# Kernel optimization log

Hardware: AMD Instinct MI355X
Metric: run time of the kernel (lower is better)

The kernel has to match this reference:

```python
import jax, jax.numpy as jnp
import numpy as np

GAMMA = 0.99
GAE_LAMBDA = 0.95
CLIP = 0.2
ENT_COEF = 0.01
VF_COEF = 0.5


def setup_inputs() -> dict:
    key = jax.random.key(0)
    ks = jax.random.split(key, 12)
    T, D, H, A = 65536, 512, 256, 16
    obs = jax.random.normal(ks[0], (T, D), dtype=jnp.float32)
    actions = jax.random.randint(ks[1], (T,), 0, A, dtype=jnp.int32)
    logprobs = jax.random.normal(ks[2], (T,), dtype=jnp.float32)
    rewards = jax.random.normal(ks[3], (T,), dtype=jnp.float32)
    terms = jax.random.uniform(ks[4], (T,), dtype=jnp.float32)
    values = jax.random.normal(ks[5], (T,), dtype=jnp.float32)
    # orthogonal-init-like scaling (std sqrt(2) for trunk, 0.01 actor, 1.0 critic)
    W1 = jax.random.normal(ks[6], (D, H), dtype=jnp.float32) * np.float32(np.sqrt(2.0 / D))
    b1 = jnp.zeros((H,), jnp.float32)
    W2 = jax.random.normal(ks[7], (H, H), dtype=jnp.float32) * np.float32(np.sqrt(2.0 / H))
    b2 = jnp.zeros((H,), jnp.float32)
    Wa = jax.random.normal(ks[8], (H, A), dtype=jnp.float32) * np.float32(0.01 / np.sqrt(H))
    ba = jnp.zeros((A,), jnp.float32)
    Wc = jax.random.normal(ks[9], (H, 1), dtype=jnp.float32) * np.float32(1.0 / np.sqrt(H))
    bc = jnp.zeros((1,), jnp.float32)
    return {"obs": obs, "actions": actions, "logprobs": logprobs, "rewards": rewards,
            "terms": terms, "values": values, "W1": W1, "b1": b1, "W2": W2, "b2": b2,
            "Wa": Wa, "ba": ba, "Wc": Wc, "bc": bc}


def reference(obs, actions, logprobs, rewards, terms, values,
              W1, b1, W2, b2, Wa, ba, Wc, bc):
    # ---- GAE (torch.no_grad in original -> stop_gradient) ----
    nonterm = 1.0 - terms                                   # [T]
    next_vals = jnp.concatenate([values[1:], jnp.zeros((1,), values.dtype)])
    delta = rewards + GAMMA * next_vals * nonterm - values  # [T]

    def step(carry, x):  # reverse recurrence a_t = d_t + g*l*nt_t * a_{t+1}
        d, nt = x
        g = d + GAMMA * GAE_LAMBDA * nt * carry
        return g, g

    _, adv = jax.lax.scan(step, jnp.float32(0.0), (delta, nonterm), reverse=True)
    adv = jax.lax.stop_gradient(adv)
    returns = adv + jax.lax.stop_gradient(values)
    vals_old = jax.lax.stop_gradient(values)

    # ---- actor-critic MLP (get_action_and_value) ----
    hidden = jnp.tanh(jnp.tanh(obs @ W1 + b1) @ W2 + b2)    # [T,256]
    logits = hidden @ Wa + ba                               # [T,A]
    logp = jax.nn.log_softmax(logits, axis=-1)
    newlp = jnp.take_along_axis(logp, actions[:, None].astype(jnp.int32), axis=1)[:, 0]
    entropy = -jnp.sum(jnp.exp(logp) * logp, axis=-1)       # [T]
    value = (hidden @ Wc + bc)[:, 0]                        # [T]

    # ---- clipped PPO losses (single full-batch minibatch) ----
    ratio = jnp.exp(newlp - logprobs)
    a = (adv - adv.mean()) / (adv.std() + 1e-8)
    pg_loss = jnp.maximum(-a * ratio, -a * jnp.clip(ratio, 1.0 - CLIP, 1.0 + CLIP)).mean()
    v_clipped = vals_old + jnp.clip(value - vals_old, -CLIP, CLIP)
    v_loss = 0.5 * jnp.maximum((value - returns) ** 2, (v_clipped - returns) ** 2).mean()
    loss = pg_loss - ENT_COEF * entropy.mean() + VF_COEF * v_loss
    return loss
```

## Files before the change

kernel.cpp:

```cpp
#include <hip/hip_runtime.h>


#define TT 65536

typedef float f32x4 __attribute__((ext_vector_type(4)));
typedef __bf16 bf16x8 __attribute__((ext_vector_type(8)));
typedef unsigned short u16x8 __attribute__((ext_vector_type(8)));
typedef unsigned int u32x4 __attribute__((ext_vector_type(4)));

__device__ __forceinline__ unsigned short f2bf(float f) {
    unsigned int u = __float_as_uint(f);
    unsigned int r = (u + 0x7fffu + ((u >> 16) & 1u)) >> 16;
    return (unsigned short)r;
}

__device__ __forceinline__ unsigned int cvt_pk_bf16(float a, float b) {
    unsigned int r;
    asm("v_cvt_pk_bf16_f32 %0, %1, %2" : "=v"(r) : "v"(a), "v"(b));
    return r;
}

__device__ __forceinline__ float fast_tanh(float x) {
    float e = __expf(2.0f * x);
    return fmaf(-2.0f, __builtin_amdgcn_rcpf(e + 1.0f), 1.0f);
}

__device__ __forceinline__ void lds_barrier() {
    asm volatile("s_waitcnt lgkmcnt(0)" ::: "memory");
    __builtin_amdgcn_s_barrier();
}

__device__ __forceinline__ void suffix_scan256(float* sC, float* sD, int i) {
    float c = sC[i], d = sD[i];
#pragma unroll
    for (int s = 1; s < 256; s <<= 1) {
        float c2 = 1.0f, d2 = 0.0f;
        if (i + s < 256) { c2 = sC[i + s]; d2 = sD[i + s]; }
        __syncthreads();
        d = d + c * d2;
        c = c * c2;
        sC[i] = c; sD[i] = d;
        __syncthreads();
    }
}

__device__ __forceinline__ void gae_cd(const float* rewards, const float* terms,
                                       const float* values, int t, float* c, float* d) {
    float nt = 1.0f - terms[t];
    float nv = (t + 1 < TT) ? values[t + 1] : 0.0f;
    *d = rewards[t] + 0.99f * nv * nt - values[t];
    *c = 0.99f * 0.95f * nt;
}

__global__ void k_prep_gae1(const float* __restrict__ W1, const float* __restrict__ W2,
                            const float* __restrict__ Wa, const float* __restrict__ Wc,
                            unsigned short* __restrict__ W1Tf, unsigned short* __restrict__ W2Tf,
                            unsigned short* __restrict__ Wavf,
                            const float* __restrict__ rewards, const float* __restrict__ terms,
                            const float* __restrict__ values, float* __restrict__ aggC,
                            float* __restrict__ aggD) {
    if (blockIdx.x < 800) {
        int idx = blockIdx.x * 256 + threadIdx.x;
        if (idx < 131072) {
            int e = idx & 7, l = (idx >> 3) & 63, nt = (idx >> 9) & 15, kt = idx >> 13;
            int col = nt * 16 + (l & 15);
            int k = kt * 32 + ((l >> 4) << 3) + e;
            W1Tf[idx] = f2bf(W1[k * 256 + col]);
        } else if (idx < 196608) {
            int i = idx - 131072;
            int e = i & 7, l = (i >> 3) & 63, nt = (i >> 9) & 15, kt = i >> 13;
            int col = nt * 16 + (l & 15);
            int k = kt * 32 + ((l >> 4) << 3) + e;
            W2Tf[i] = f2bf(W2[k * 256 + col]);
        } else if (idx < 204800) {
            int i = idx - 196608;
            int e = i & 7, l = (i >> 3) & 63, h = (i >> 9) & 1, kt = i >> 10;
            int k = kt * 32 + ((l >> 4) << 3) + e;
            int a = l & 15;
            float v = (h == 0) ? Wa[k * 16 + a] : ((a == 0) ? Wc[k] : 0.0f);
            Wavf[i] = f2bf(v);
        }
        return;
    }
    __shared__ float sC[256], sD[256];
    int i = threadIdx.x;
    int b = blockIdx.x - 800;
    int t = b * 256 + i;
    float c, d;
    gae_cd(rewards, terms, values, t, &c, &d);
    sC[i] = c; sD[i] = d;
    __syncthreads();
    suffix_scan256(sC, sD, i);
    if (i == 0) { aggC[b] = sC[0]; aggD[b] = sD[0]; }
}

__global__ void k_gae3(const float* __restrict__ rewards, const float* __restrict__ terms,
                       const float* __restrict__ values, const float* __restrict__ aggC,
                       const float* __restrict__ aggD, float* __restrict__ adv,
                       float* __restrict__ ret, float* __restrict__ sumP) {
    __shared__ float sC[256], sD[256];
    int i = threadIdx.x, b = blockIdx.x;
    sC[i] = aggC[i]; sD[i] = aggD[i];
    __syncthreads();
    suffix_scan256(sC, sD, i);
    float carry = (b < 255) ? sD[b + 1] : 0.0f;
    __syncthreads();

    int t = b * 256 + i;
    float c, d;
    gae_cd(rewards, terms, values, t, &c, &d);
    sC[i] = c; sD[i] = d;
    __syncthreads();
    suffix_scan256(sC, sD, i);
    float a = sD[i] + sC[i] * carry;
    adv[t] = a;
    ret[t] = a + values[t];
    __syncthreads();
    sC[i] = a; sD[i] = a * a;
    __syncthreads();
#pragma unroll
    for (int s = 128; s > 0; s >>= 1) {
        if (i < s) { sC[i] += sC[i + s]; sD[i] += sD[i + s]; }
        __syncthreads();
    }
    if (i == 0) { sumP[2 * b] = sC[0]; sumP[2 * b + 1] = sD[0]; }
}

__global__ void k_gae4(const float* __restrict__ sumP, float* __restrict__ stats) {
    __shared__ float s1[256], s2[256];
    int i = threadIdx.x;
    s1[i] = sumP[2 * i]; s2[i] = sumP[2 * i + 1];
    __syncthreads();
#pragma unroll
    for (int s = 128; s > 0; s >>= 1) {
        if (i < s) { s1[i] += s1[i + s]; s2[i] += s2[i + s]; }
        __syncthreads();
    }
    if (i == 0) {
        float mean = s1[0] * (1.0f / TT);
        float var = s2[0] * (1.0f / TT) - mean * mean;
        stats[0] = mean;
        stats[1] = 1.0f / (sqrtf(fmaxf(var, 0.0f)) + 1e-8f);
    }
}

__global__ __launch_bounds__(256, 3) void k_mlp(
    const float* __restrict__ obs, const int* __restrict__ actions,
    const float* __restrict__ logprobs, const float* __restrict__ values,
    const float* __restrict__ b1, const float* __restrict__ b2,
    const float* __restrict__ ba, const float* __restrict__ bc,
    const unsigned short* __restrict__ W1Tf, const unsigned short* __restrict__ W2Tf,
    const unsigned short* __restrict__ Wavf, const float* __restrict__ adv,
    const float* __restrict__ ret, const float* __restrict__ stats,
    float* __restrict__ lossP) {
    __shared__ __align__(16) unsigned char SM[40960];
    unsigned short* smA = (unsigned short*)SM;
    unsigned short* smH = (unsigned short*)(SM + 8192);

    const int tid = threadIdx.x;
    const int wid = tid >> 6;
    const int lane = tid & 63;
    const int cl = lane & 15;
    const int gg = lane >> 4;
    const int bm0 = blockIdx.x * 64;

    const int arow = tid >> 2;
    const int aslot = tid & 3;
    const int adst = arow * 32 + ((aslot ^ ((arow >> 1) & 3)) << 3);
    const float* aSrc = obs + (size_t)(bm0 + arow) * 512 + aslot * 8;

    const float meanA = stats[0], rstdA = stats[1];

    float b1v[4], b2v[4];
#pragma unroll
    for (int n = 0; n < 4; ++n) {
        int c = wid * 64 + n * 16 + cl;
        b1v[n] = b1[c];
        b2v[n] = b2[c];
    }
    const float bav = ba[cl];
    const float bc0 = bc[0];

    f32x4 acc[4][4];
#pragma unroll
    for (int m = 0; m < 4; ++m)
#pragma unroll
        for (int n = 0; n < 4; ++n) acc[m][n] = (f32x4){0.f, 0.f, 0.f, 0.f};

    auto cvtWriteA = [&](const float4& f0, const float4& f1, int buf) {
        u32x4 pk;
        pk[0] = cvt_pk_bf16(f0.x, f0.y);
        pk[1] = cvt_pk_bf16(f0.z, f0.w);
        pk[2] = cvt_pk_bf16(f1.x, f1.y);
        pk[3] = cvt_pk_bf16(f1.z, f1.w);
        *(u32x4*)&smA[buf * 2048 + adst] = pk;
    };

    {
        const unsigned short* bBase = W1Tf + ((size_t)(wid * 4) << 9) + lane * 8;
        float4 pa0[3], pa1[3];
#pragma unroll
        for (int p = 0; p < 3; ++p) {
            pa0[p] = *(const float4*)(aSrc + p * 32);
            pa1[p] = *(const float4*)(aSrc + p * 32 + 4);
        }
        cvtWriteA(pa0[0], pa1[0], 0);
        lds_barrier();
#pragma unroll
        for (int t = 0; t < 16; ++t) {
            if (t < 13) {
                pa0[t % 3] = *(const float4*)(aSrc + (t + 3) * 32);
                pa1[t % 3] = *(const float4*)(aSrc + (t + 3) * 32 + 4);
            }
            bf16x8 av[4], bv[4];
#pragma unroll
            for (int n = 0; n < 4; ++n)
                bv[n] = *(const bf16x8*)(bBase + ((size_t)(t * 16 + n) << 9));
#pragma unroll
            for (int m = 0; m < 4; ++m) {
                int ra = m * 16 + cl;
                av[m] = *(const bf16x8*)&smA[(t & 1) * 2048 + ra * 32 + ((gg ^ ((ra >> 1) & 3)) << 3)];
            }
#pragma unroll
            for (int m = 0; m < 4; ++m)
#pragma unroll
                for (int n = 0; n < 4; ++n)
                    acc[m][n] = __builtin_amdgcn_mfma_f32_16x16x32_bf16(av[m], bv[n], acc[m][n], 0, 0, 0);
            if (t < 15) cvtWriteA(pa0[(t + 1) % 3], pa1[(t + 1) % 3], (t + 1) & 1);
            lds_barrier();
        }
    }

#pragma unroll
    for (int m = 0; m < 4; ++m)
#pragma unroll
        for (int n = 0; n < 4; ++n)
#pragma unroll
            for (int j = 0; j < 4; ++j) {
                int r = m * 16 + gg * 4 + j;
                int c = wid * 64 + n * 16 + cl;
                smH[r * 256 + (c ^ ((r & 7) << 3))] = f2bf(fast_tanh(acc[m][n][j] + b1v[n]));
                acc[m][n][j] = 0.0f;
            }
    __syncthreads();

    {
        const unsigned short* bBase = W2Tf + ((size_t)(wid * 4) << 9) + lane * 8;
#pragma unroll
        for (int t = 0; t < 8; ++t) {
            bf16x8 av[4], bv[4];
#pragma unroll
            for (int n = 0; n < 4; ++n)
                bv[n] = *(const bf16x8*)(bBase + ((size_t)(t * 16 + n) << 9));
#pragma unroll
            for (int m = 0; m < 4; ++m) {
                int ra = m * 16 + cl;
                av[m] = *(const bf16x8*)&smH[ra * 256 + ((t * 32 + gg * 8) ^ ((ra & 7) << 3))];
            }
#pragma unroll
            for (int m = 0; m < 4; ++m)
#pragma unroll
                for (int n = 0; n < 4; ++n)
                    acc[m][n] = __builtin_amdgcn_mfma_f32_16x16x32_bf16(av[m], bv[n], acc[m][n], 0, 0, 0);
        }
    }

    __syncthreads();
#pragma unroll
    for (int m = 0; m < 4; ++m)
#pragma unroll
        for (int n = 0; n < 4; ++n)
#pragma unroll
            for (int j = 0; j < 4; ++j) {
                int r = m * 16 + gg * 4 + j;
                int c = wid * 64 + n * 16 + cl;
                smH[r * 256 + (c ^ ((r & 7) << 3))] = f2bf(fast_tanh(acc[m][n][j] + b2v[n]));
            }
    __syncthreads();

    float lsum = 0.0f;
    {
        f32x4 acc_a = {0.f, 0.f, 0.f, 0.f}, acc_v = {0.f, 0.f, 0.f, 0.f};
        const unsigned short* wBase = Wavf + lane * 8;
#pragma unroll
        for (int kk = 0; kk < 8; ++kk) {
            int r = wid * 16 + cl;
            bf16x8 av = *(const bf16x8*)&smH[r * 256 + ((kk * 32 + gg * 8) ^ ((r & 7) << 3))];
            bf16x8 bva = *(const bf16x8*)(wBase + ((size_t)(kk * 2) << 9));
            bf16x8 bvv = *(const bf16x8*)(wBase + ((size_t)(kk * 2 + 1) << 9));
            acc_a = __builtin_amdgcn_mfma_f32_16x16x32_bf16(av, bva, acc_a, 0, 0, 0);
            acc_v = __builtin_amdgcn_mfma_f32_16x16x32_bf16(av, bvv, acc_v, 0, 0, 0);
        }

        const int t0 = bm0 + wid * 16;
#pragma unroll
        for (int j = 0; j < 4; ++j) {
            int t = t0 + gg * 4 + j;
            float lg = acc_a[j] + bav;
            float mx = lg;
#pragma unroll
            for (int dd = 1; dd < 16; dd <<= 1) mx = fmaxf(mx, __shfl_xor(mx, dd));
            float ex = __expf(lg - mx);
            float se = ex;
#pragma unroll
            for (int dd = 1; dd < 16; dd <<= 1) se += __shfl_xor(se, dd);
            float ls = __logf(se);
            float lp = lg - mx - ls;
            float pl = __expf(lp) * lp;
            float ent = pl;
#pragma unroll
            for (int dd = 1; dd < 16; dd <<= 1) ent += __shfl_xor(ent, dd);
            ent = -ent;
            int act = actions[t];
            float newlp = __shfl(lp, (lane & 48) | act);
            float val = __shfl(acc_v[j], lane & 48) + bc0;

            float lpo = logprobs[t];
            float at = (adv[t] - meanA) * rstdA;
            float rt = ret[t];
            float vo = values[t];
            float ratio = __expf(newlp - lpo);
            float rcl = fminf(fmaxf(ratio, 0.8f), 1.2f);
            float pg = fmaxf(-at * ratio, -at * rcl);
            float vcl = vo + fminf(fmaxf(val - vo, -0.2f), 0.2f);
            float dv = val - rt, dvc = vcl - rt;
            float vl = fmaxf(dv * dv, dvc * dvc);
            if (cl == 0) lsum += pg - 0.01f * ent + 0.25f * vl;
        }
        lsum += __shfl_xor(lsum, 16);
        lsum += __shfl_xor(lsum, 32);
    }
    __syncthreads();
    float* red2 = (float*)SM;
    if (lane == 0) red2[wid] = lsum;
    __syncthreads();
    if (tid == 0) lossP[blockIdx.x] = red2[0] + red2[1] + red2[2] + red2[3];
}

__global__ void k_final(const float* __restrict__ lossP, float* __restrict__ out) {
    __shared__ float s[256];
    int i = threadIdx.x;
    s[i] = lossP[i] + lossP[i + 256] + lossP[i + 512] + lossP[i + 768];
    __syncthreads();
#pragma unroll
    for (int st = 128; st > 0; st >>= 1) {
        if (i < st) s[i] += s[i + st];
        __syncthreads();
    }
    if (i == 0) out[0] = s[0] * (1.0f / TT);
}

extern "C" void kernel_launch(void* const* d_in, const int* in_sizes, int n_in,
                              void* d_out, int out_size, void* d_ws, size_t ws_size,
                              hipStream_t stream) {
    const float* obs      = (const float*)d_in[0];
    const int*   actions  = (const int*)d_in[1];
    const float* logprobs = (const float*)d_in[2];
    const float* rewards  = (const float*)d_in[3];
    const float* terms    = (const float*)d_in[4];
    const float* values   = (const float*)d_in[5];
    const float* W1 = (const float*)d_in[6];
    const float* b1 = (const float*)d_in[7];
    const float* W2 = (const float*)d_in[8];
    const float* b2 = (const float*)d_in[9];
    const float* Wa = (const float*)d_in[10];
    const float* ba = (const float*)d_in[11];
    const float* Wc = (const float*)d_in[12];
    const float* bc = (const float*)d_in[13];

    char* ws = (char*)d_ws;
    unsigned short* W1Tf = (unsigned short*)(ws + 0);
    unsigned short* W2Tf = (unsigned short*)(ws + 262144);
    unsigned short* Wavf = (unsigned short*)(ws + 393216);
    float* advp  = (float*)(ws + 409600);
    float* retp  = (float*)(ws + 671744);
    float* aggC  = (float*)(ws + 933888);
    float* aggD  = (float*)(ws + 934912);
    float* sumP  = (float*)(ws + 936960);
    float* stats = (float*)(ws + 939008);
    float* lossP = (float*)(ws + 939072);

    k_prep_gae1<<<1056, 256, 0, stream>>>(W1, W2, Wa, Wc, W1Tf, W2Tf, Wavf,
                                          rewards, terms, values, aggC, aggD);
    k_gae3<<<256, 256, 0, stream>>>(rewards, terms, values, aggC, aggD, advp, retp, sumP);
    k_gae4<<<1, 256, 0, stream>>>(sumP, stats);
    k_mlp<<<1024, 256, 0, stream>>>(obs, actions, logprobs, values, b1, b2, ba, bc,
                                    W1Tf, W2Tf, Wavf, advp, retp, stats, lossP);
    k_final<<<1, 256, 0, stream>>>(lossP, (float*)d_out);
}
```

Baseline: 73.42 us.

## Stage full obs tile in LDS upfront and prefetch first weight tiles

```diff
diff --git a/kernel.cpp b/kernel.cpp
--- a/kernel.cpp
+++ b/kernel.cpp
@@ -62,23 +62,29 @@
     if (blockIdx.x < 800) {
         int idx = blockIdx.x * 256 + threadIdx.x;
         if (idx < 131072) {
-            int e = idx & 7, l = (idx >> 3) & 63, nt = (idx >> 9) & 15, kt = idx >> 13;
-            int col = nt * 16 + (l & 15);
-            int k = kt * 32 + ((l >> 4) << 3) + e;
-            W1Tf[idx] = f2bf(W1[k * 256 + col]);
+            int col = idx & 255, k = idx >> 8;
+            int kt = k >> 5, lh = (k & 31) >> 3, e = k & 7;
+            int nt = col >> 4, cl = col & 15;
+            W1Tf[(((kt * 16 + nt) * 64) + lh * 16 + cl) * 8 + e] = f2bf(W1[k * 256 + col]);
         } else if (idx < 196608) {
             int i = idx - 131072;
-            int e = i & 7, l = (i >> 3) & 63, nt = (i >> 9) & 15, kt = i >> 13;
-            int col = nt * 16 + (l & 15);
-            int k = kt * 32 + ((l >> 4) << 3) + e;
-            W2Tf[i] = f2bf(W2[k * 256 + col]);
+            int col = i & 255, k = i >> 8;
+            int kt = k >> 5, lh = (k & 31) >> 3, e = k & 7;
+            int nt = col >> 4, cl = col & 15;
+            W2Tf[(((kt * 16 + nt) * 64) + lh * 16 + cl) * 8 + e] = f2bf(W2[k * 256 + col]);
         } else if (idx < 204800) {
             int i = idx - 196608;
-            int e = i & 7, l = (i >> 3) & 63, h = (i >> 9) & 1, kt = i >> 10;
-            int k = kt * 32 + ((l >> 4) << 3) + e;
-            int a = l & 15;
-            float v = (h == 0) ? Wa[k * 16 + a] : ((a == 0) ? Wc[k] : 0.0f);
-            Wavf[i] = f2bf(v);
+            if (i < 4096) {
+                int a = i & 15, k = i >> 4;
+                int kt = k >> 5, lh = (k & 31) >> 3, e = k & 7;
+                Wavf[(((kt * 2 + 0) * 64) + lh * 16 + a) * 8 + e] = f2bf(Wa[k * 16 + a]);
+            } else {
+                int j = i - 4096;
+                int a = j & 15, k = j >> 4;
+                int kt = k >> 5, lh = (k & 31) >> 3, e = k & 7;
+                float v = (a == 0) ? Wc[k] : 0.0f;
+                Wavf[(((kt * 2 + 1) * 64) + lh * 16 + a) * 8 + e] = f2bf(v);
+            }
         }
         return;
     }
@@ -144,7 +150,7 @@
     }
 }
 
-__global__ __launch_bounds__(256, 3) void k_mlp(
+__global__ __launch_bounds__(256, 2) void k_mlp(
     const float* __restrict__ obs, const int* __restrict__ actions,
     const float* __restrict__ logprobs, const float* __restrict__ values,
     const float* __restrict__ b1, const float* __restrict__ b2,
@@ -153,9 +159,9 @@
     const unsigned short* __restrict__ Wavf, const float* __restrict__ adv,
     const float* __restrict__ ret, const float* __restrict__ stats,
     float* __restrict__ lossP) {
-    __shared__ __align__(16) unsigned char SM[40960];
+    __shared__ __align__(16) unsigned char SM[65536];
     unsigned short* smA = (unsigned short*)SM;
-    unsigned short* smH = (unsigned short*)(SM + 8192);
+    unsigned short* smH = (unsigned short*)SM;
 
     const int tid = threadIdx.x;
     const int wid = tid >> 6;
@@ -164,11 +170,6 @@
     const int gg = lane >> 4;
     const int bm0 = blockIdx.x * 64;
 
-    const int arow = tid >> 2;
-    const int aslot = tid & 3;
-    const int adst = arow * 32 + ((aslot ^ ((arow >> 1) & 3)) << 3);
-    const float* aSrc = obs + (size_t)(bm0 + arow) * 512 + aslot * 8;
-
     const float meanA = stats[0], rstdA = stats[1];
 
     float b1v[4], b2v[4];
@@ -181,55 +182,64 @@
     const float bav = ba[cl];
     const float bc0 = bc[0];
 
+    {
+        const int arow = tid >> 2;
+        const int acl4 = (tid & 3) * 8;
+        const int axor = (arow & 7) << 3;
+        const float* aSrc = obs + (size_t)(bm0 + arow) * 512 + acl4;
+        unsigned short* aDst = smA + arow * 512;
+#pragma unroll
+        for (int ct = 0; ct < 16; ++ct) {
+            float4 f0 = *(const float4*)(aSrc + ct * 32);
+            float4 f1 = *(const float4*)(aSrc + ct * 32 + 4);
+            u32x4 pk;
+            pk[0] = cvt_pk_bf16(f0.x, f0.y);
+            pk[1] = cvt_pk_bf16(f0.z, f0.w);
+            pk[2] = cvt_pk_bf16(f1.x, f1.y);
+            pk[3] = cvt_pk_bf16(f1.z, f1.w);
+            *(u32x4*)&aDst[(ct * 32 + acl4) ^ axor] = pk;
+        }
+    }
+
     f32x4 acc[4][4];
 #pragma unroll
     for (int m = 0; m < 4; ++m)
 #pragma unroll
         for (int n = 0; n < 4; ++n) acc[m][n] = (f32x4){0.f, 0.f, 0.f, 0.f};
 
-    auto cvtWriteA = [&](const float4& f0, const float4& f1, int buf) {
-        u32x4 pk;
-        pk[0] = cvt_pk_bf16(f0.x, f0.y);
-        pk[1] = cvt_pk_bf16(f0.z, f0.w);
-        pk[2] = cvt_pk_bf16(f1.x, f1.y);
-        pk[3] = cvt_pk_bf16(f1.z, f1.w);
-        *(u32x4*)&smA[buf * 2048 + adst] = pk;
-    };
-
-    {
-        const unsigned short* bBase = W1Tf + ((size_t)(wid * 4) << 9) + lane * 8;
-        float4 pa0[3], pa1[3];
-#pragma unroll
-        for (int p = 0; p < 3; ++p) {
-            pa0[p] = *(const float4*)(aSrc + p * 32);
-            pa1[p] = *(const float4*)(aSrc + p * 32 + 4);
-        }
-        cvtWriteA(pa0[0], pa1[0], 0);
-        lds_barrier();
-#pragma unroll
-        for (int t = 0; t < 16; ++t) {
-            if (t < 13) {
-                pa0[t % 3] = *(const float4*)(aSrc + (t + 3) * 32);
-                pa1[t % 3] = *(const float4*)(aSrc + (t + 3) * 32 + 4);
-            }
-            bf16x8 av[4], bv[4];
+    const unsigned short* b1Base = W1Tf + ((size_t)(wid * 4) << 9) + lane * 8;
+    bf16x8 bv0[4];
+#pragma unroll
+    for (int n = 0; n < 4; ++n)
+        bv0[n] = *(const bf16x8*)(b1Base + ((size_t)n << 9));
+
+    lds_barrier();
+
+#pragma unroll
+    for (int t = 0; t < 16; ++t) {
+        bf16x8 av[4], bv[4];
+#pragma unroll
+        for (int n = 0; n < 4; ++n)
+            bv[n] = (t == 0) ? bv0[n]
+                             : *(const bf16x8*)(b1Base + ((size_t)(t * 16 + n) << 9));
+#pragma unroll
+        for (int m = 0; m < 4; ++m) {
+            int ra = m * 16 + cl;
+            av[m] = *(const bf16x8*)&smA[ra * 512 + ((t * 32 + gg * 8) ^ ((ra & 7) << 3))];
+        }
+#pragma unroll
+        for (int m = 0; m < 4; ++m)
 #pragma unroll
             for (int n = 0; n < 4; ++n)
-                bv[n] = *(const bf16x8*)(bBase + ((size_t)(t * 16 + n) << 9));
-#pragma unroll
-            for (int m = 0; m < 4; ++m) {
-                int ra = m * 16 + cl;
-                av[m] = *(const bf16x8*)&smA[(t & 1) * 2048 + ra * 32 + ((gg ^ ((ra >> 1) & 3)) << 3)];
-            }
-#pragma unroll
-            for (int m = 0; m < 4; ++m)
-#pragma unroll
-                for (int n = 0; n < 4; ++n)
-                    acc[m][n] = __builtin_amdgcn_mfma_f32_16x16x32_bf16(av[m], bv[n], acc[m][n], 0, 0, 0);
-            if (t < 15) cvtWriteA(pa0[(t + 1) % 3], pa1[(t + 1) % 3], (t + 1) & 1);
-            lds_barrier();
-        }
-    }
+                acc[m][n] = __builtin_amdgcn_mfma_f32_16x16x32_bf16(av[m], bv[n], acc[m][n], 0, 0, 0);
+    }
+
+    const unsigned short* b2Base = W2Tf + ((size_t)(wid * 4) << 9) + lane * 8;
+#pragma unroll
+    for (int n = 0; n < 4; ++n)
+        bv0[n] = *(const bf16x8*)(b2Base + ((size_t)n << 9));
+
+    lds_barrier();
 
 #pragma unroll
     for (int m = 0; m < 4; ++m)
@@ -242,30 +252,29 @@
                 smH[r * 256 + (c ^ ((r & 7) << 3))] = f2bf(fast_tanh(acc[m][n][j] + b1v[n]));
                 acc[m][n][j] = 0.0f;
             }
-    __syncthreads();
-
-    {
-        const unsigned short* bBase = W2Tf + ((size_t)(wid * 4) << 9) + lane * 8;
-#pragma unroll
-        for (int t = 0; t < 8; ++t) {
-            bf16x8 av[4], bv[4];
+    lds_barrier();
+
+#pragma unroll
+    for (int t = 0; t < 8; ++t) {
+        bf16x8 av[4], bv[4];
+#pragma unroll
+        for (int n = 0; n < 4; ++n)
+            bv[n] = (t == 0) ? bv0[n]
+                             : *(const bf16x8*)(b2Base + ((size_t)(t * 16 + n) << 9));
+#pragma unroll
+        for (int m = 0; m < 4; ++m) {
+            int ra = m * 16 + cl;
+            av[m] = *(const bf16x8*)&smH[ra * 256 + ((t * 32 + gg * 8) ^ ((ra & 7) << 3))];
+        }
+#pragma unroll
+        for (int m = 0; m < 4; ++m)
 #pragma unroll
             for (int n = 0; n < 4; ++n)
-                bv[n] = *(const bf16x8*)(bBase + ((size_t)(t * 16 + n) << 9));
-#pragma unroll
-            for (int m = 0; m < 4; ++m) {
-                int ra = m * 16 + cl;
-                av[m] = *(const bf16x8*)&smH[ra * 256 + ((t * 32 + gg * 8) ^ ((ra & 7) << 3))];
-            }
-#pragma unroll
-            for (int m = 0; m < 4; ++m)
-#pragma unroll
-                for (int n = 0; n < 4; ++n)
-                    acc[m][n] = __builtin_amdgcn_mfma_f32_16x16x32_bf16(av[m], bv[n], acc[m][n], 0, 0, 0);
-        }
-    }
-
-    __syncthreads();
+                acc[m][n] = __builtin_amdgcn_mfma_f32_16x16x32_bf16(av[m], bv[n], acc[m][n], 0, 0, 0);
+    }
+
+    lds_barrier();
+
 #pragma unroll
     for (int m = 0; m < 4; ++m)
 #pragma unroll
@@ -276,7 +285,7 @@
                 int c = wid * 64 + n * 16 + cl;
                 smH[r * 256 + (c ^ ((r & 7) << 3))] = f2bf(fast_tanh(acc[m][n][j] + b2v[n]));
             }
-    __syncthreads();
+    lds_barrier();
 
     float lsum = 0.0f;
     {
@@ -330,10 +339,10 @@
         lsum += __shfl_xor(lsum, 16);
         lsum += __shfl_xor(lsum, 32);
     }
-    __syncthreads();
+    lds_barrier();
     float* red2 = (float*)SM;
     if (lane == 0) red2[wid] = lsum;
-    __syncthreads();
+    lds_barrier();
     if (tid == 0) lossP[blockIdx.x] = red2[0] + red2[1] + red2[2] + red2[3];
 }
 
```

After: 67.50 us. 1.09x faster.
